# Performance work log

Hardware: AMD Instinct MI355X
Metric: run time of the kernel (lower is better)

The kernel has to match this reference:

```python
import jax, jax.numpy as jnp
import numpy as np

N_NODES = 50000
N_EDGES = 150000
N_TRIS = 100000
F = 256
L = 4


def setup_inputs() -> dict:
    key = jax.random.key(0)
    ks = jax.random.split(key, 8)
    x = jax.random.normal(ks[0], (N_EDGES, F), dtype=jnp.float32)
    edge_nodes = jax.random.randint(ks[1], (N_EDGES, 2), 0, N_NODES)
    tri_edges = jax.random.randint(ks[2], (N_TRIS, 3), 0, N_EDGES)
    tri_signs = (jax.random.randint(ks[3], (N_TRIS, 3), 0, 2) * 2 - 1).astype(jnp.int32)
    std = float(np.sqrt(2.0 / (F + F)))  # xavier_uniform-equivalent std
    W0_stack = jax.random.normal(ks[4], (L, F, F), dtype=jnp.float32) * std
    W1_stack = jax.random.normal(ks[5], (L, F, F), dtype=jnp.float32) * std
    W2_stack = jax.random.normal(ks[6], (L, F, F), dtype=jnp.float32) * std
    W0_L = jax.random.normal(ks[7], (F, 1), dtype=jnp.float32) * float(np.sqrt(2.0 / (F + 1)))
    return {"x": x, "W0_stack": W0_stack, "W1_stack": W1_stack, "W2_stack": W2_stack,
            "W0_L": W0_L, "edge_nodes": edge_nodes, "tri_edges": tri_edges, "tri_signs": tri_signs}


def _b1_mm(edge_nodes, y):
    # B1 @ y : [E,F] -> [N,F];  B1[u,e] = -1, B1[v,e] = +1
    u, v = edge_nodes[:, 0], edge_nodes[:, 1]
    out = jnp.zeros((N_NODES, y.shape[1]), y.dtype)
    return out.at[u].add(-y).at[v].add(y)


def _b1t_mm(edge_nodes, z):
    # B1.T @ z : [N,F] -> [E,F]
    return z[edge_nodes[:, 1]] - z[edge_nodes[:, 0]]


def _b2t_mm(tri_edges, signs, y):
    # B2.T @ y : [E,F] -> [T,F]
    return jnp.einsum('tkf,tk->tf', y[tri_edges], signs)


def _b2_mm(tri_edges, signs, w):
    # B2 @ w : [T,F] -> [E,F]
    contrib = w[:, None, :] * signs[:, :, None]  # [T,3,F]
    out = jnp.zeros((N_EDGES, w.shape[1]), w.dtype)
    return out.at[tri_edges.reshape(-1)].add(contrib.reshape(-1, w.shape[1]))


def reference(x, W0_stack, W1_stack, W2_stack, W0_L, edge_nodes, tri_edges, tri_signs):
    signs = tri_signs.astype(x.dtype)
    for i in range(L):
        d2 = _b2_mm(tri_edges, signs, _b2t_mm(tri_edges, signs, x @ W2_stack[i]))
        d1 = x @ W1_stack[i]
        d0 = _b1t_mm(edge_nodes, _b1_mm(edge_nodes, x @ W0_stack[i]))
        x = jax.nn.relu(d2 + d1 + d0)
    return _b1_mm(edge_nodes, x @ W0_L)  # [N_NODES, 1]
```

## Files before the change

kernel.cpp:

```cpp
#include <hip/hip_runtime.h>

#define M_EDGES 150000
#define NN_NODES 50000
#define N_TRIS  100000
#define F 256
#define NLAYERS 4

#define T0 1172
#define T1 391
#define T2 782
#define NTILES (T0 + T1 + T2)
#define NT_PAD 2352

typedef __attribute__((ext_vector_type(8))) __bf16 bf16x8;
typedef __attribute__((ext_vector_type(4))) float f32x4;

__device__ inline unsigned short f2bf(float f) {
    unsigned int u = __float_as_uint(f);
    u += 0x7fff + ((u >> 16) & 1);
    return (unsigned short)(u >> 16);
}
__device__ inline float bf2f(unsigned short h) {
    return __uint_as_float(((unsigned int)h) << 16);
}

__device__ inline void async16(const void* g, void* l) {
    __builtin_amdgcn_global_load_lds(
        (const __attribute__((address_space(1))) void*)g,
        (__attribute__((address_space(3))) void*)l, 16, 0, 0);
}

__global__ __launch_bounds__(256) void gemm_mfma(
    const unsigned short* __restrict__ xb,
    const unsigned short* __restrict__ sb,
    const unsigned short* __restrict__ qb,
    const unsigned short* __restrict__ wt,
    unsigned short* __restrict__ y1,
    unsigned short* __restrict__ zb,
    unsigned short* __restrict__ wb)
{
    __shared__ unsigned short As[128 * 32];
    __shared__ unsigned short Bs[128 * 32];

    const int b    = blockIdx.x;
    const int xcd  = b & 7;
    const int c    = b >> 3;
    const int tile = (c >> 1) * 8 + xcd;
    const int bn   = c & 1;
    if (tile >= NTILES) return;

    int seg, tloc;
    if (tile < T0)            { seg = 0; tloc = tile; }
    else if (tile < T0 + T1)  { seg = 1; tloc = tile - T0; }
    else                      { seg = 2; tloc = tile - T0 - T1; }
    const unsigned short* Asrc = (seg == 0) ? xb : (seg == 1) ? sb : qb;
    const int nrows = (seg == 0) ? M_EDGES : (seg == 1) ? NN_NODES : N_TRIS;
    const unsigned short* wsel = wt + seg * 65536;
    unsigned short* dst = (seg == 0) ? y1 : (seg == 1) ? zb : wb;

    const int tid  = threadIdx.x;
    const int bm0  = tloc * 128;
    const int wid  = tid >> 6;
    const int lane = tid & 63;
    const int lm   = lane & 15;
    const int lh   = lane >> 4;
    const int wm   = wid >> 1;
    const int wn   = wid & 1;
    const int wbase = tid & ~63;

    f32x4 cacc[4][4];
#pragma unroll
    for (int i = 0; i < 4; i++)
#pragma unroll
        for (int j = 0; j < 4; j++) cacc[i][j] = (f32x4){0.f, 0.f, 0.f, 0.f};

    for (int k0 = 0; k0 < 256; k0 += 32) {
#pragma unroll
        for (int s = 0; s < 2; s++) {
            int i   = s * 256 + tid;
            int row = i >> 2;
            int g   = (i & 3) ^ ((row >> 1) & 3);
            int gr  = bm0 + row;
            if (gr > nrows - 1) gr = nrows - 1;
            async16(Asrc + (size_t)gr * 256 + k0 + g * 8,
                    As + (size_t)(s * 256 + wbase) * 8);
            int nrow = bn * 128 + row;
            async16(wsel + (size_t)nrow * 256 + k0 + g * 8,
                    Bs + (size_t)(s * 256 + wbase) * 8);
        }
        asm volatile("s_waitcnt vmcnt(0)" ::: "memory");
        __syncthreads();

        bf16x8 a[4], bfr[4];
#pragma unroll
        for (int i = 0; i < 4; i++) {
            int rr = wm * 64 + i * 16 + lm;
            a[i] = *(const bf16x8*)(As + rr * 32 + ((lh ^ ((rr >> 1) & 3)) * 8));
        }
#pragma unroll
        for (int j = 0; j < 4; j++) {
            int rr = wn * 64 + j * 16 + lm;
            bfr[j] = *(const bf16x8*)(Bs + rr * 32 + ((lh ^ ((rr >> 1) & 3)) * 8));
        }
#pragma unroll
        for (int i = 0; i < 4; i++)
#pragma unroll
            for (int j = 0; j < 4; j++)
                cacc[i][j] = __builtin_amdgcn_mfma_f32_16x16x32_bf16(bfr[j], a[i], cacc[i][j], 0, 0, 0);
        __syncthreads();
    }

#pragma unroll
    for (int i = 0; i < 4; i++) {
        int grow = bm0 + wm * 64 + i * 16 + lm;
        if (grow < nrows) {
#pragma unroll
            for (int j = 0; j < 4; j++) {
                int col = bn * 128 + wn * 64 + j * 16 + lh * 4;
                ushort4 r;
                r.x = f2bf(cacc[i][j][0]);
                r.y = f2bf(cacc[i][j][1]);
                r.z = f2bf(cacc[i][j][2]);
                r.w = f2bf(cacc[i][j][3]);
                *(ushort4*)(dst + (size_t)grow * 256 + col) = r;
            }
        }
    }
}

__global__ __launch_bounds__(256) void count_nodes(
    const int* __restrict__ en, int* __restrict__ cnt)
{
    int e = blockIdx.x * 256 + threadIdx.x;
    if (e < M_EDGES) {
        atomicAdd(&cnt[en[2 * e]], 1);
        atomicAdd(&cnt[en[2 * e + 1]], 1);
    }
}

__global__ __launch_bounds__(256) void count_tris(
    const int* __restrict__ te, int* __restrict__ cnt)
{
    int t = blockIdx.x * 256 + threadIdx.x;
    if (t < N_TRIS) {
#pragma unroll
        for (int k = 0; k < 3; k++) atomicAdd(&cnt[te[3 * t + k]], 1);
    }
}

__global__ __launch_bounds__(256) void scan_block(
    const int* __restrict__ cnt, int* __restrict__ off,
    int* __restrict__ partial, int n)
{
    __shared__ int s[256];
    int t = threadIdx.x;
    int gid = blockIdx.x * 256 + t;
    int v = (gid < n) ? cnt[gid] : 0;
    s[t] = v;
    __syncthreads();
    for (int o = 1; o < 256; o <<= 1) {
        int x = (t >= o) ? s[t - o] : 0;
        __syncthreads();
        s[t] += x;
        __syncthreads();
    }
    if (gid < n) off[gid] = s[t] - v;
    if (t == 255) partial[blockIdx.x] = s[255];
}

__global__ __launch_bounds__(1024) void scan_partial(int* __restrict__ partial, int nb)
{
    __shared__ int s[1024];
    int t = threadIdx.x;
    int v = (t < nb) ? partial[t] : 0;
    s[t] = v;
    __syncthreads();
    for (int o = 1; o < 1024; o <<= 1) {
        int x = (t >= o) ? s[t - o] : 0;
        __syncthreads();
        s[t] += x;
        __syncthreads();
    }
    if (t < nb) partial[t] = s[t] - v;
}

__global__ __launch_bounds__(256) void scan_add(
    int* __restrict__ off, int* __restrict__ cursor,
    const int* __restrict__ partial, int n, int total)
{
    int gid = blockIdx.x * 256 + threadIdx.x;
    if (gid == 0) off[n] = total;
    if (gid < n) {
        int o = off[gid] + partial[blockIdx.x];
        off[gid] = o;
        cursor[gid] = o;
    }
}

__global__ __launch_bounds__(256) void fill_nodes(
    const int* __restrict__ en, int* __restrict__ cursor, int* __restrict__ adj)
{
    int e = blockIdx.x * 256 + threadIdx.x;
    if (e < M_EDGES) {
        int u = en[2 * e], v = en[2 * e + 1];
        adj[atomicAdd(&cursor[u], 1)] = (e << 1);
        adj[atomicAdd(&cursor[v], 1)] = (e << 1) | 1;
    }
}

__global__ __launch_bounds__(256) void fill_tris(
    const int* __restrict__ te, const int* __restrict__ ts,
    int* __restrict__ cursor, int* __restrict__ adj)
{
    int t = blockIdx.x * 256 + threadIdx.x;
    if (t < N_TRIS) {
#pragma unroll
        for (int k = 0; k < 3; k++) {
            int e = te[3 * t + k];
            int neg = (ts[3 * t + k] < 0) ? 1 : 0;
            adj[atomicAdd(&cursor[e], 1)] = (t << 1) | neg;
        }
    }
}

#define ZN_BLOCKS (NN_NODES / 4)
#define WT_BLOCKS (N_TRIS / 4)

__global__ __launch_bounds__(256) void agg_fused(
    const unsigned short* __restrict__ xb,
    const int* __restrict__ noff,
    const int* __restrict__ nadj,
    unsigned short* __restrict__ sbuf,
    const int* __restrict__ te,
    const int* __restrict__ ts,
    unsigned short* __restrict__ qbuf)
{
    int lane = threadIdx.x & 63;
    int f = lane * 4;
    if (blockIdx.x < ZN_BLOCKS) {
        int n = blockIdx.x * 4 + (threadIdx.x >> 6);
        int beg = noff[n], end = noff[n + 1];
        float ax = 0.f, ay = 0.f, az = 0.f, aw = 0.f;
        int i = beg;
        for (; i + 1 < end; i += 2) {
            int ea = nadj[i], eb = nadj[i + 1];
            float sa = (ea & 1) ? 1.f : -1.f;
            float sgb = (eb & 1) ? 1.f : -1.f;
            ushort4 va = *(const ushort4*)(xb + (size_t)(ea >> 1) * 256 + f);
            ushort4 vb = *(const ushort4*)(xb + (size_t)(eb >> 1) * 256 + f);
            ax += sa * bf2f(va.x) + sgb * bf2f(vb.x);
            ay += sa * bf2f(va.y) + sgb * bf2f(vb.y);
            az += sa * bf2f(va.z) + sgb * bf2f(vb.z);
            aw += sa * bf2f(va.w) + sgb * bf2f(vb.w);
        }
        if (i < end) {
            int ea = nadj[i];
            float sa = (ea & 1) ? 1.f : -1.f;
            ushort4 va = *(const ushort4*)(xb + (size_t)(ea >> 1) * 256 + f);
            ax += sa * bf2f(va.x);
            ay += sa * bf2f(va.y);
            az += sa * bf2f(va.z);
            aw += sa * bf2f(va.w);
        }
        ushort4 r;
        r.x = f2bf(ax); r.y = f2bf(ay); r.z = f2bf(az); r.w = f2bf(aw);
        *(ushort4*)(sbuf + (size_t)n * 256 + f) = r;
    } else {
        int t = (blockIdx.x - ZN_BLOCKS) * 4 + (threadIdx.x >> 6);
        int e0 = te[3 * t + 0], e1 = te[3 * t + 1], e2 = te[3 * t + 2];
        float s0 = (float)ts[3 * t + 0];
        float s1 = (float)ts[3 * t + 1];
        float s2 = (float)ts[3 * t + 2];
        ushort4 a4 = *(const ushort4*)(xb + (size_t)e0 * 256 + f);
        ushort4 b4 = *(const ushort4*)(xb + (size_t)e1 * 256 + f);
        ushort4 d4 = *(const ushort4*)(xb + (size_t)e2 * 256 + f);
        ushort4 r;
        r.x = f2bf(s0 * bf2f(a4.x) + s1 * bf2f(b4.x) + s2 * bf2f(d4.x));
        r.y = f2bf(s0 * bf2f(a4.y) + s1 * bf2f(b4.y) + s2 * bf2f(d4.y));
        r.z = f2bf(s0 * bf2f(a4.z) + s1 * bf2f(b4.z) + s2 * bf2f(d4.z));
        r.w = f2bf(s0 * bf2f(a4.w) + s1 * bf2f(b4.w) + s2 * bf2f(d4.w));
        *(ushort4*)(qbuf + (size_t)t * 256 + f) = r;
    }
}

__global__ __launch_bounds__(256) void relu_fused(
    const unsigned short* __restrict__ y1,
    const unsigned short* __restrict__ w,
    const unsigned short* __restrict__ z,
    const int* __restrict__ en,
    const int* __restrict__ eoff,
    const int* __restrict__ eadj,
    unsigned short* __restrict__ xb)
{
    int e = blockIdx.x * 4 + (threadIdx.x >> 6);
    int lane = threadIdx.x & 63;
    int f = lane * 4;
    int u = en[2 * e], v = en[2 * e + 1];
    int beg = eoff[e], end = eoff[e + 1];
    ushort4 a4 = *(const ushort4*)(y1 + (size_t)e * 256 + f);
    ushort4 zv = *(const ushort4*)(z + (size_t)v * 256 + f);
    ushort4 zu = *(const ushort4*)(z + (size_t)u * 256 + f);
    float sx = bf2f(a4.x) + bf2f(zv.x) - bf2f(zu.x);
    float sy = bf2f(a4.y) + bf2f(zv.y) - bf2f(zu.y);
    float sz = bf2f(a4.z) + bf2f(zv.z) - bf2f(zu.z);
    float sw = bf2f(a4.w) + bf2f(zv.w) - bf2f(zu.w);
    int i = beg;
    for (; i + 1 < end; i += 2) {
        int ta = eadj[i], tb = eadj[i + 1];
        float sa = (ta & 1) ? -1.f : 1.f;
        float sgb = (tb & 1) ? -1.f : 1.f;
        ushort4 wa = *(const ushort4*)(w + (size_t)(ta >> 1) * 256 + f);
        ushort4 wbv = *(const ushort4*)(w + (size_t)(tb >> 1) * 256 + f);
        sx += sa * bf2f(wa.x) + sgb * bf2f(wbv.x);
        sy += sa * bf2f(wa.y) + sgb * bf2f(wbv.y);
        sz += sa * bf2f(wa.z) + sgb * bf2f(wbv.z);
        sw += sa * bf2f(wa.w) + sgb * bf2f(wbv.w);
    }
    if (i < end) {
        int ta = eadj[i];
        float sa = (ta & 1) ? -1.f : 1.f;
        ushort4 wa = *(const ushort4*)(w + (size_t)(ta >> 1) * 256 + f);
        sx += sa * bf2f(wa.x);
        sy += sa * bf2f(wa.y);
        sz += sa * bf2f(wa.z);
        sw += sa * bf2f(wa.w);
    }
    ushort4 r;
    r.x = f2bf(fmaxf(sx, 0.f));
    r.y = f2bf(fmaxf(sy, 0.f));
    r.z = f2bf(fmaxf(sz, 0.f));
    r.w = f2bf(fmaxf(sw, 0.f));
    *(ushort4*)(xb + (size_t)e * 256 + f) = r;
}

__global__ __launch_bounds__(256) void dotp(
    const unsigned short* __restrict__ xb,
    const float* __restrict__ wl,
    float* __restrict__ p)
{
    int e = blockIdx.x * 4 + (threadIdx.x >> 6);
    int lane = threadIdx.x & 63;
    ushort4 xv = *(const ushort4*)(xb + (size_t)e * 256 + lane * 4);
    float4 wv = *(const float4*)(wl + lane * 4);
    float s = bf2f(xv.x) * wv.x + bf2f(xv.y) * wv.y +
              bf2f(xv.z) * wv.z + bf2f(xv.w) * wv.w;
#pragma unroll
    for (int off = 32; off > 0; off >>= 1)
        s += __shfl_down(s, off, 64);
    if (lane == 0) p[e] = s;
}

__global__ __launch_bounds__(256) void out_nodes(
    const float* __restrict__ p,
    const int* __restrict__ noff,
    const int* __restrict__ nadj,
    float* __restrict__ out)
{
    int n = blockIdx.x * 256 + threadIdx.x;
    if (n >= NN_NODES) return;
    int beg = noff[n], end = noff[n + 1];
    float s = 0.f;
    for (int i = beg; i < end; i++) {
        int ent = nadj[i];
        float sg = (ent & 1) ? 1.f : -1.f;
        s += sg * p[ent >> 1];
    }
    out[n] = s;
}

__global__ __launch_bounds__(256) void cvt_x(
    const float* __restrict__ x, unsigned short* __restrict__ xb)
{
    int idx = blockIdx.x * 256 + threadIdx.x;
    float4 v = *(const float4*)(x + (size_t)idx * 4);
    ushort4 r;
    r.x = f2bf(v.x); r.y = f2bf(v.y); r.z = f2bf(v.z); r.w = f2bf(v.w);
    *(ushort4*)(xb + (size_t)idx * 4) = r;
}

__global__ __launch_bounds__(256) void cvt_w(
    const float* __restrict__ W0, const float* __restrict__ W1,
    const float* __restrict__ W2, unsigned short* __restrict__ wt)
{
    int idx = blockIdx.x * 256 + threadIdx.x;
    int l = idx / (3 * 65536);
    int rem = idx - l * (3 * 65536);
    int seg = rem >> 16;
    int n = (rem >> 8) & 255;
    int k = rem & 255;
    const float* src = (seg == 0) ? W1 : (seg == 1) ? W0 : W2;
    wt[idx] = f2bf(src[(size_t)l * 65536 + k * 256 + n]);
}

extern "C" void kernel_launch(void* const* d_in, const int* in_sizes, int n_in,
                              void* d_out, int out_size, void* d_ws, size_t ws_size,
                              hipStream_t stream)
{
    const float* x0  = (const float*)d_in[0];
    const float* W0s = (const float*)d_in[1];
    const float* W1s = (const float*)d_in[2];
    const float* W2s = (const float*)d_in[3];
    const float* WL  = (const float*)d_in[4];
    const int*   en  = (const int*)d_in[5];
    const int*   te  = (const int*)d_in[6];
    const int*   ts  = (const int*)d_in[7];
    float* out = (float*)d_out;

    const size_t MF = (size_t)M_EDGES * F;
    unsigned short* xb = (unsigned short*)d_ws;
    unsigned short* y1 = xb + MF;
    unsigned short* sbuf = y1 + MF;
    unsigned short* qbuf = sbuf + (size_t)NN_NODES * 256;
    unsigned short* wt = qbuf + (size_t)N_TRIS * 256;
    unsigned short* wb = wt + (size_t)4 * 3 * 65536;
    unsigned short* zb = wb + (size_t)N_TRIS * 256;
    float* p = (float*)(zb + (size_t)NN_NODES * 256);
    int* noff = (int*)(p + M_EDGES);
    int* ncur = noff + (NN_NODES + 1);
    int* nadj = ncur + NN_NODES;
    int* eoff = nadj + 2 * M_EDGES;
    int* ecur = eoff + (M_EDGES + 1);
    int* eadj = ecur + M_EDGES;
    int* part = eadj + 3 * N_TRIS;

    cvt_w<<<(4 * 3 * 65536) / 256, 256, 0, stream>>>(W0s, W1s, W2s, wt);
    cvt_x<<<(int)(MF / 4 / 256), 256, 0, stream>>>(x0, xb);

    const int nbN = (NN_NODES + 255) / 256;
    const int nbE = (M_EDGES + 255) / 256;
    hipMemsetAsync(ncur, 0, NN_NODES * sizeof(int), stream);
    hipMemsetAsync(ecur, 0, M_EDGES * sizeof(int), stream);
    count_nodes<<<nbE, 256, 0, stream>>>(en, ncur);
    count_tris<<<(N_TRIS + 255) / 256, 256, 0, stream>>>(te, ecur);
    scan_block<<<nbN, 256, 0, stream>>>(ncur, noff, part, NN_NODES);
    scan_partial<<<1, 1024, 0, stream>>>(part, nbN);
    scan_add<<<nbN, 256, 0, stream>>>(noff, ncur, part, NN_NODES, 2 * M_EDGES);
    fill_nodes<<<nbE, 256, 0, stream>>>(en, ncur, nadj);
    scan_block<<<nbE, 256, 0, stream>>>(ecur, eoff, part, M_EDGES);
    scan_partial<<<1, 1024, 0, stream>>>(part, nbE);
    scan_add<<<nbE, 256, 0, stream>>>(eoff, ecur, part, M_EDGES, 3 * N_TRIS);
    fill_tris<<<(N_TRIS + 255) / 256, 256, 0, stream>>>(te, ts, ecur, eadj);

    const int gemm_blocks = NT_PAD * 2;
    for (int l = 0; l < NLAYERS; l++) {
        agg_fused<<<ZN_BLOCKS + WT_BLOCKS, 256, 0, stream>>>(
            xb, noff, nadj, sbuf, te, ts, qbuf);
        gemm_mfma<<<gemm_blocks, 256, 0, stream>>>(
            xb, sbuf, qbuf, wt + (size_t)l * 3 * 65536, y1, zb, wb);
        relu_fused<<<M_EDGES / 4, 256, 0, stream>>>(y1, wb, zb, en, eoff, eadj, xb);
    }

    dotp<<<M_EDGES / 4, 256, 0, stream>>>(xb, WL, p);
    out_nodes<<<(NN_NODES + 255) / 256, 256, 0, stream>>>(p, noff, nadj, out);
}
```

Measured before the change: 1.241 ms.

## Co-schedule x@W1 GEMM with sparse aggregation in one launch, split remaining GEMMs

The edge-feature GEMM (x@W1), which depends only on x, now runs in the same kernel launch as the node and triangle gather aggregations. The two GEMMs that depend on those aggregations go into a separate kernel. This overlaps the memory-bound gathers with the compute-bound GEMM tiles and removes some tail idle time. In exchange, every fused_a block reserves GEMM shared memory, which may lower occupancy for the gather blocks, and mixing the two workloads changes the cache behaviour.

```diff
diff --git a/kernel.cpp b/kernel.cpp
--- a/kernel.cpp
+++ b/kernel.cpp
@@ -9,8 +9,14 @@
 #define T0 1172
 #define T1 391
 #define T2 782
-#define NTILES (T0 + T1 + T2)
-#define NT_PAD 2352
+#define T0_PAD 1176
+#define G0_BLOCKS (T0_PAD * 2)
+#define T12 (T1 + T2)
+#define T12_PAD 1176
+#define G12_BLOCKS (T12_PAD * 2)
+
+#define ZN_BLOCKS (NN_NODES / 4)
+#define WT_BLOCKS (N_TRIS / 4)
 
 typedef __attribute__((ext_vector_type(8))) __bf16 bf16x8;
 typedef __attribute__((ext_vector_type(4))) float f32x4;
@@ -30,34 +36,13 @@
         (__attribute__((address_space(3))) void*)l, 16, 0, 0);
 }
 
-__global__ __launch_bounds__(256) void gemm_mfma(
-    const unsigned short* __restrict__ xb,
-    const unsigned short* __restrict__ sb,
-    const unsigned short* __restrict__ qb,
-    const unsigned short* __restrict__ wt,
-    unsigned short* __restrict__ y1,
-    unsigned short* __restrict__ zb,
-    unsigned short* __restrict__ wb)
-{
-    __shared__ unsigned short As[128 * 32];
-    __shared__ unsigned short Bs[128 * 32];
-
-    const int b    = blockIdx.x;
-    const int xcd  = b & 7;
-    const int c    = b >> 3;
-    const int tile = (c >> 1) * 8 + xcd;
-    const int bn   = c & 1;
-    if (tile >= NTILES) return;
-
-    int seg, tloc;
-    if (tile < T0)            { seg = 0; tloc = tile; }
-    else if (tile < T0 + T1)  { seg = 1; tloc = tile - T0; }
-    else                      { seg = 2; tloc = tile - T0 - T1; }
-    const unsigned short* Asrc = (seg == 0) ? xb : (seg == 1) ? sb : qb;
-    const int nrows = (seg == 0) ? M_EDGES : (seg == 1) ? NN_NODES : N_TRIS;
-    const unsigned short* wsel = wt + seg * 65536;
-    unsigned short* dst = (seg == 0) ? y1 : (seg == 1) ? zb : wb;
-
+__device__ inline void gemm_tile_body(
+    const unsigned short* __restrict__ Asrc, int nrows,
+    const unsigned short* __restrict__ wseg,
+    unsigned short* __restrict__ dst,
+    int tloc, int bn,
+    unsigned short* As, unsigned short* Bs)
+{
     const int tid  = threadIdx.x;
     const int bm0  = tloc * 128;
     const int wid  = tid >> 6;
@@ -85,7 +70,7 @@
             async16(Asrc + (size_t)gr * 256 + k0 + g * 8,
                     As + (size_t)(s * 256 + wbase) * 8);
             int nrow = bn * 128 + row;
-            async16(wsel + (size_t)nrow * 256 + k0 + g * 8,
+            async16(wseg + (size_t)nrow * 256 + k0 + g * 8,
                     Bs + (size_t)(s * 256 + wbase) * 8);
         }
         asm volatile("s_waitcnt vmcnt(0)" ::: "memory");
@@ -128,106 +113,10 @@
     }
 }
 
-__global__ __launch_bounds__(256) void count_nodes(
-    const int* __restrict__ en, int* __restrict__ cnt)
-{
-    int e = blockIdx.x * 256 + threadIdx.x;
-    if (e < M_EDGES) {
-        atomicAdd(&cnt[en[2 * e]], 1);
-        atomicAdd(&cnt[en[2 * e + 1]], 1);
-    }
-}
-
-__global__ __launch_bounds__(256) void count_tris(
-    const int* __restrict__ te, int* __restrict__ cnt)
-{
-    int t = blockIdx.x * 256 + threadIdx.x;
-    if (t < N_TRIS) {
-#pragma unroll
-        for (int k = 0; k < 3; k++) atomicAdd(&cnt[te[3 * t + k]], 1);
-    }
-}
-
-__global__ __launch_bounds__(256) void scan_block(
-    const int* __restrict__ cnt, int* __restrict__ off,
-    int* __restrict__ partial, int n)
-{
-    __shared__ int s[256];
-    int t = threadIdx.x;
-    int gid = blockIdx.x * 256 + t;
-    int v = (gid < n) ? cnt[gid] : 0;
-    s[t] = v;
-    __syncthreads();
-    for (int o = 1; o < 256; o <<= 1) {
-        int x = (t >= o) ? s[t - o] : 0;
-        __syncthreads();
-        s[t] += x;
-        __syncthreads();
-    }
-    if (gid < n) off[gid] = s[t] - v;
-    if (t == 255) partial[blockIdx.x] = s[255];
-}
-
-__global__ __launch_bounds__(1024) void scan_partial(int* __restrict__ partial, int nb)
-{
-    __shared__ int s[1024];
-    int t = threadIdx.x;
-    int v = (t < nb) ? partial[t] : 0;
-    s[t] = v;
-    __syncthreads();
-    for (int o = 1; o < 1024; o <<= 1) {
-        int x = (t >= o) ? s[t - o] : 0;
-        __syncthreads();
-        s[t] += x;
-        __syncthreads();
-    }
-    if (t < nb) partial[t] = s[t] - v;
-}
-
-__global__ __launch_bounds__(256) void scan_add(
-    int* __restrict__ off, int* __restrict__ cursor,
-    const int* __restrict__ partial, int n, int total)
-{
-    int gid = blockIdx.x * 256 + threadIdx.x;
-    if (gid == 0) off[n] = total;
-    if (gid < n) {
-        int o = off[gid] + partial[blockIdx.x];
-        off[gid] = o;
-        cursor[gid] = o;
-    }
-}
-
-__global__ __launch_bounds__(256) void fill_nodes(
-    const int* __restrict__ en, int* __restrict__ cursor, int* __restrict__ adj)
-{
-    int e = blockIdx.x * 256 + threadIdx.x;
-    if (e < M_EDGES) {
-        int u = en[2 * e], v = en[2 * e + 1];
-        adj[atomicAdd(&cursor[u], 1)] = (e << 1);
-        adj[atomicAdd(&cursor[v], 1)] = (e << 1) | 1;
-    }
-}
-
-__global__ __launch_bounds__(256) void fill_tris(
-    const int* __restrict__ te, const int* __restrict__ ts,
-    int* __restrict__ cursor, int* __restrict__ adj)
-{
-    int t = blockIdx.x * 256 + threadIdx.x;
-    if (t < N_TRIS) {
-#pragma unroll
-        for (int k = 0; k < 3; k++) {
-            int e = te[3 * t + k];
-            int neg = (ts[3 * t + k] < 0) ? 1 : 0;
-            adj[atomicAdd(&cursor[e], 1)] = (t << 1) | neg;
-        }
-    }
-}
-
-#define ZN_BLOCKS (NN_NODES / 4)
-#define WT_BLOCKS (N_TRIS / 4)
-
-__global__ __launch_bounds__(256) void agg_fused(
+__global__ __launch_bounds__(256) void fused_a(
     const unsigned short* __restrict__ xb,
+    const unsigned short* __restrict__ wt,
+    unsigned short* __restrict__ y1,
     const int* __restrict__ noff,
     const int* __restrict__ nadj,
     unsigned short* __restrict__ sbuf,
@@ -235,10 +124,24 @@
     const int* __restrict__ ts,
     unsigned short* __restrict__ qbuf)
 {
+    __shared__ unsigned short As[128 * 32];
+    __shared__ unsigned short Bs[128 * 32];
+
+    const int b = blockIdx.x;
+    if (b < G0_BLOCKS) {
+        const int xcd = b & 7;
+        const int c   = b >> 3;
+        const int tile = (c >> 1) * 8 + xcd;
+        const int bn   = c & 1;
+        if (tile >= T0) return;
+        gemm_tile_body(xb, M_EDGES, wt, y1, tile, bn, As, Bs);
+        return;
+    }
     int lane = threadIdx.x & 63;
     int f = lane * 4;
-    if (blockIdx.x < ZN_BLOCKS) {
-        int n = blockIdx.x * 4 + (threadIdx.x >> 6);
+    int gb = b - G0_BLOCKS;
+    if (gb < ZN_BLOCKS) {
+        int n = gb * 4 + (threadIdx.x >> 6);
         int beg = noff[n], end = noff[n + 1];
         float ax = 0.f, ay = 0.f, az = 0.f, aw = 0.f;
         int i = beg;
@@ -266,7 +169,7 @@
         r.x = f2bf(ax); r.y = f2bf(ay); r.z = f2bf(az); r.w = f2bf(aw);
         *(ushort4*)(sbuf + (size_t)n * 256 + f) = r;
     } else {
-        int t = (blockIdx.x - ZN_BLOCKS) * 4 + (threadIdx.x >> 6);
+        int t = (gb - ZN_BLOCKS) * 4 + (threadIdx.x >> 6);
         int e0 = te[3 * t + 0], e1 = te[3 * t + 1], e2 = te[3 * t + 2];
         float s0 = (float)ts[3 * t + 0];
         float s1 = (float)ts[3 * t + 1];
@@ -280,6 +183,124 @@
         r.z = f2bf(s0 * bf2f(a4.z) + s1 * bf2f(b4.z) + s2 * bf2f(d4.z));
         r.w = f2bf(s0 * bf2f(a4.w) + s1 * bf2f(b4.w) + s2 * bf2f(d4.w));
         *(ushort4*)(qbuf + (size_t)t * 256 + f) = r;
+    }
+}
+
+__global__ __launch_bounds__(256) void gemm12(
+    const unsigned short* __restrict__ sb,
+    const unsigned short* __restrict__ qb,
+    const unsigned short* __restrict__ wt,
+    unsigned short* __restrict__ zb,
+    unsigned short* __restrict__ wb)
+{
+    __shared__ unsigned short As[128 * 32];
+    __shared__ unsigned short Bs[128 * 32];
+
+    const int b    = blockIdx.x;
+    const int xcd  = b & 7;
+    const int c    = b >> 3;
+    const int tile = (c >> 1) * 8 + xcd;
+    const int bn   = c & 1;
+    if (tile >= T12) return;
+
+    if (tile < T1)
+        gemm_tile_body(sb, NN_NODES, wt + 65536, zb, tile, bn, As, Bs);
+    else
+        gemm_tile_body(qb, N_TRIS, wt + 131072, wb, tile - T1, bn, As, Bs);
+}
+
+__global__ __launch_bounds__(256) void count_nodes(
+    const int* __restrict__ en, int* __restrict__ cnt)
+{
+    int e = blockIdx.x * 256 + threadIdx.x;
+    if (e < M_EDGES) {
+        atomicAdd(&cnt[en[2 * e]], 1);
+        atomicAdd(&cnt[en[2 * e + 1]], 1);
+    }
+}
+
+__global__ __launch_bounds__(256) void count_tris(
+    const int* __restrict__ te, int* __restrict__ cnt)
+{
+    int t = blockIdx.x * 256 + threadIdx.x;
+    if (t < N_TRIS) {
+#pragma unroll
+        for (int k = 0; k < 3; k++) atomicAdd(&cnt[te[3 * t + k]], 1);
+    }
+}
+
+__global__ __launch_bounds__(256) void scan_block(
+    const int* __restrict__ cnt, int* __restrict__ off,
+    int* __restrict__ partial, int n)
+{
+    __shared__ int s[256];
+    int t = threadIdx.x;
+    int gid = blockIdx.x * 256 + t;
+    int v = (gid < n) ? cnt[gid] : 0;
+    s[t] = v;
+    __syncthreads();
+    for (int o = 1; o < 256; o <<= 1) {
+        int x = (t >= o) ? s[t - o] : 0;
+        __syncthreads();
+        s[t] += x;
+        __syncthreads();
+    }
+    if (gid < n) off[gid] = s[t] - v;
+    if (t == 255) partial[blockIdx.x] = s[255];
+}
+
+__global__ __launch_bounds__(1024) void scan_partial(int* __restrict__ partial, int nb)
+{
+    __shared__ int s[1024];
+    int t = threadIdx.x;
+    int v = (t < nb) ? partial[t] : 0;
+    s[t] = v;
+    __syncthreads();
+    for (int o = 1; o < 1024; o <<= 1) {
+        int x = (t >= o) ? s[t - o] : 0;
+        __syncthreads();
+        s[t] += x;
+        __syncthreads();
+    }
+    if (t < nb) partial[t] = s[t] - v;
+}
+
+__global__ __launch_bounds__(256) void scan_add(
+    int* __restrict__ off, int* __restrict__ cursor,
+    const int* __restrict__ partial, int n, int total)
+{
+    int gid = blockIdx.x * 256 + threadIdx.x;
+    if (gid == 0) off[n] = total;
+    if (gid < n) {
+        int o = off[gid] + partial[blockIdx.x];
+        off[gid] = o;
+        cursor[gid] = o;
+    }
+}
+
+__global__ __launch_bounds__(256) void fill_nodes(
+    const int* __restrict__ en, int* __restrict__ cursor, int* __restrict__ adj)
+{
+    int e = blockIdx.x * 256 + threadIdx.x;
+    if (e < M_EDGES) {
+        int u = en[2 * e], v = en[2 * e + 1];
+        adj[atomicAdd(&cursor[u], 1)] = (e << 1);
+        adj[atomicAdd(&cursor[v], 1)] = (e << 1) | 1;
+    }
+}
+
+__global__ __launch_bounds__(256) void fill_tris(
+    const int* __restrict__ te, const int* __restrict__ ts,
+    int* __restrict__ cursor, int* __restrict__ adj)
+{
+    int t = blockIdx.x * 256 + threadIdx.x;
+    if (t < N_TRIS) {
+#pragma unroll
+        for (int k = 0; k < 3; k++) {
+            int e = te[3 * t + k];
+            int neg = (ts[3 * t + k] < 0) ? 1 : 0;
+            adj[atomicAdd(&cursor[e], 1)] = (t << 1) | neg;
+        }
     }
 }
 
@@ -441,12 +462,12 @@
     scan_add<<<nbE, 256, 0, stream>>>(eoff, ecur, part, M_EDGES, 3 * N_TRIS);
     fill_tris<<<(N_TRIS + 255) / 256, 256, 0, stream>>>(te, ts, ecur, eadj);
 
-    const int gemm_blocks = NT_PAD * 2;
+    const int fa_blocks = G0_BLOCKS + ZN_BLOCKS + WT_BLOCKS;
     for (int l = 0; l < NLAYERS; l++) {
-        agg_fused<<<ZN_BLOCKS + WT_BLOCKS, 256, 0, stream>>>(
-            xb, noff, nadj, sbuf, te, ts, qbuf);
-        gemm_mfma<<<gemm_blocks, 256, 0, stream>>>(
-            xb, sbuf, qbuf, wt + (size_t)l * 3 * 65536, y1, zb, wb);
+        const unsigned short* wl_ = wt + (size_t)l * 3 * 65536;
+        fused_a<<<fa_blocks, 256, 0, stream>>>(
+            xb, wl_, y1, noff, nadj, sbuf, te, ts, qbuf);
+        gemm12<<<G12_BLOCKS, 256, 0, stream>>>(sbuf, qbuf, wl_, zb, wb);
         relu_fused<<<M_EDGES / 4, 256, 0, stream>>>(y1, wb, zb, en, eoff, eadj, xb);
     }
 
```

New measurement: 2.131 ms. 1.72x slower.
